# Kernel tuning notes

Hardware: AMD Instinct MI355X
Metric: run time of the kernel (lower is better)

Reference implementation:

```python
import jax, jax.numpy as jnp
import numpy as np

B, N, NG, K, H, C, BD = 4, 2048, 12, 16, 64, 128, 64
M = N // 4  # fps with down_sample=4
TWO_PI = 2.0 * np.pi


def _knn_idx(q, x, k):
    # q [Q,3] queries, x [P,3] pool -> [Q,k] indices of k nearest points in x
    d2 = jnp.sum((q[:, None, :] - x[None, :, :]) ** 2, axis=-1)
    _, idx = jax.lax.top_k(-d2, k)
    return idx


def _fps_idx(pos, m):
    # farthest point sampling, fixed m points, start at index 0
    n = pos.shape[0]
    def body(carry, _):
        d, last = carry
        dist = jnp.sum((pos - pos[last]) ** 2, axis=-1)
        d = jnp.minimum(d, dist)
        return (d, jnp.argmax(d)), last
    (_, _), idx = jax.lax.scan(body, (jnp.full((n,), 1e10, pos.dtype), jnp.int32(0)), None, length=m)
    return idx


def _basis_mlp(z, rff_w, w1, b1, w2, b2):
    # RFF -> Linear -> GELU -> Linear -> GELU
    p = TWO_PI * (z @ rff_w)
    f = jnp.concatenate([jnp.sin(p), jnp.cos(p)], axis=-1)
    h = jax.nn.gelu(f @ w1 + b1)
    return jax.nn.gelu(h @ w2 + b2)


def _interaction(x, nbr, kbx, kbR, kx_w, kx_b, kR_w, kR_b, mix_w, mix_b):
    # depthwise separable group conv: spatial gather-multiply-mean, then orientation mix
    kx = kbx @ kx_w + kx_b                     # [M,K,NG,C] spatial depthwise kernel
    kR = kbR @ kR_w + kR_b                     # [NG,NG,C] orientation depthwise kernel
    agg = jnp.mean(x[nbr] * kx, axis=1)        # [M,NG,C] mean over K neighbors
    y = jnp.einsum('bnc,mnc->bmc', agg, kR) / kR.shape[0]
    return x + jax.nn.gelu(y @ mix_w + mix_b)


def setup_inputs():
    key = jax.random.key(0)
    ks = iter(jax.random.split(key, 64))
    def randn(shape, std=1.0):
        return std * jax.random.normal(next(ks), shape, dtype=jnp.float32)
    inp = {}
    inp['pos'] = jax.random.uniform(next(ks), (B, N, 3), dtype=jnp.float32)
    nrm = randn((B, N, 3))
    inp['normal'] = nrm / jnp.linalg.norm(nrm, axis=-1, keepdims=True)
    g = randn((NG, 3))
    inp['grid'] = g / jnp.linalg.norm(g, axis=-1, keepdims=True)
    def lin(name, fin, fout):
        inp[name + '_w'] = randn((fin, fout), 1.0 / np.sqrt(fin))
        inp[name + '_b'] = jnp.zeros((fout,), jnp.float32)
    lin('emb1', 4, H); lin('emb2', H, H)
    lin('down', H, C)
    inp['bx_rff'] = randn((2, C // 2), 10.0)   # sigma=10
    lin('bx1', C, C); lin('bx2', C, BD)
    inp['bR_rff'] = randn((1, C // 2), 10.0)
    lin('bR1', C, C); lin('bR2', C, BD)
    for j in ('i1', 'i2'):
        lin(j + '_kx', BD, C); lin(j + '_kR', BD, C); lin(j + '_mix', C, C)
    lin('post1', C, 256); lin('post2', 256, 64); lin('post3', 64, 1)
    return inp


def reference(pos, normal, grid, emb1_w, emb1_b, emb2_w, emb2_b, down_w, down_b,
              bx_rff, bx1_w, bx1_b, bx2_w, bx2_b, bR_rff, bR1_w, bR1_b, bR2_w, bR2_b,
              i1_kx_w, i1_kx_b, i1_kR_w, i1_kR_b, i1_mix_w, i1_mix_b,
              i2_kx_w, i2_kx_b, i2_kR_w, i2_kR_b, i2_mix_w, i2_mix_b,
              post1_w, post1_b, post2_w, post2_b, post3_w, post3_b):
    def per_graph(p, nm):
        # lift: fiber features = <grid, normal> plus broadcast positions -> [N,NG,4]
        feat = jnp.concatenate([(nm @ grid.T)[:, :, None],
                                jnp.broadcast_to(p[:, None, :], (p.shape[0], NG, 3))], axis=-1)
        x = jax.nn.gelu(feat @ emb1_w + emb1_b) @ emb2_w + emb2_b   # [N,NG,H]
        # downsample block: fps + knn + linear/relu + scatter-max (exactly K edges per target)
        sel = _fps_idx(p, M)
        nbr_d = _knn_idx(p[sel], p, K)                               # [M,K] into N
        h = jax.nn.relu(x @ down_w + down_b)                         # [N,NG,C]
        x = jnp.max(h[nbr_d], axis=1)                                # [M,NG,C]
        ps = p[sel]
        # convolver block: knn graph + r3s2 edge attrs + basis MLPs + 2 interaction layers
        nbr = _knn_idx(ps, ps, K)                                    # [M,K] into M
        rel = ps[nbr] - ps[:, None, :]                               # pos[src]-pos[tgt], [M,K,3]
        rz = jnp.einsum('mke,ne->mkn', rel, grid)                    # [M,K,NG]
        rxy = jnp.sqrt(jnp.sum((rel[:, :, None, :] - rz[..., None] * grid) ** 2, axis=-1) + 1e-12)
        rpx = jnp.stack([rxy, rz], axis=-1)                          # [M,K,NG,2]
        rpR = (grid @ grid.T)[:, :, None]                            # [NG,NG,1]
        kbx = _basis_mlp(rpx, bx_rff, bx1_w, bx1_b, bx2_w, bx2_b)    # [M,K,NG,BD]
        kbR = _basis_mlp(rpR, bR_rff, bR1_w, bR1_b, bR2_w, bR2_b)    # [NG,NG,BD]
        x = _interaction(x, nbr, kbx, kbR, i1_kx_w, i1_kx_b, i1_kR_w, i1_kR_b, i1_mix_w, i1_mix_b)
        x = _interaction(x, nbr, kbx, kbR, i2_kx_w, i2_kx_b, i2_kR_w, i2_kR_b, i2_mix_w, i2_mix_b)
        # readout: mean over grid, global mean pool, MLP head
        g = jnp.mean(x, axis=(0, 1))                                 # [C]
        h1 = jax.nn.gelu(g @ post1_w + post1_b)
        h2 = jax.nn.gelu(h1 @ post2_w + post2_b)
        return h2 @ post3_w + post3_b                                # [1]
    return jax.vmap(per_graph)(pos, normal)                          # [B,1]
```

## Files before the change

### kernel.cpp

```cpp
#include <hip/hip_runtime.h>
#include <hip/hip_bf16.h>
#include <cfloat>

#define B_ 4
#define N_ 2048
#define NG_ 12
#define K_ 16
#define H_ 64
#define C_ 128
#define BD_ 64
#define M_ 512

typedef __attribute__((ext_vector_type(8))) short short8;
typedef __attribute__((ext_vector_type(4))) float floatx4;
typedef unsigned short ushort_t;
typedef unsigned int uint_t;

__device__ __forceinline__ float gelu_f(float x){
  float s = 0.7978845608028654f*(x + 0.044715f*x*x*x);
  float e = __expf(2.0f*s);
  float t = 1.0f - 2.0f/(e + 1.0f);
  return 0.5f*x*(1.0f + t);
}

__device__ __forceinline__ ushort_t bf16_rne(float x){
  uint_t u = __float_as_uint(x);
  uint_t r = (u + 0x7fffu + ((u >> 16) & 1u)) >> 16;
  return (ushort_t)r;
}

__device__ __forceinline__ uint_t pack_hl(float x){
  ushort_t hi = bf16_rne(x);
  float hif = __uint_as_float(((uint_t)hi)<<16);
  ushort_t lo = bf16_rne(x - hif);
  return (uint_t)hi | ((uint_t)lo << 16);
}

__device__ __forceinline__ uint_t cvtpk_bf16(float a, float b){
  uint_t r;
  asm("v_cvt_pk_bf16_f32 %0, %1, %2" : "=v"(r) : "v"(a), "v"(b));
  return r;
}

__device__ __forceinline__ void split2(float v0, float v1, uint_t& hp, uint_t& lp){
  hp = cvtpk_bf16(v0, v1);
  float h0 = __uint_as_float(hp << 16);
  float h1 = __uint_as_float(hp & 0xffff0000u);
  lp = cvtpk_bf16(v0 - h0, v1 - h1);
}

__device__ __forceinline__ uint_t pack_hl2(float v){
  uint_t hp = cvtpk_bf16(v, v);
  float hf = __uint_as_float(hp << 16);
  uint_t lp = cvtpk_bf16(v - hf, v - hf);
  return (hp & 0xffffu) | (lp << 16);
}

__device__ __forceinline__ uint_t perm_lo16(uint_t a, uint_t b){ return __builtin_amdgcn_perm(a, b, 0x05040100u); }
__device__ __forceinline__ uint_t perm_hi16(uint_t a, uint_t b){ return __builtin_amdgcn_perm(a, b, 0x07060302u); }

#define UNPACK8(Q0, Q1, AH, AL) { \
  uint_t* _ap = (uint_t*)&(AH); uint_t* _lp = (uint_t*)&(AL); \
  _ap[0] = perm_lo16((Q0).y, (Q0).x); _ap[1] = perm_lo16((Q0).w, (Q0).z); \
  _ap[2] = perm_lo16((Q1).y, (Q1).x); _ap[3] = perm_lo16((Q1).w, (Q1).z); \
  _lp[0] = perm_hi16((Q0).y, (Q0).x); _lp[1] = perm_hi16((Q0).w, (Q0).z); \
  _lp[2] = perm_hi16((Q1).y, (Q1).x); _lp[3] = perm_hi16((Q1).w, (Q1).z); }

#define DPP_AMAX(CTRL) { \
  int _vb = __float_as_int(v); \
  int _ov = __builtin_amdgcn_update_dpp(_vb, _vb, (CTRL), 0xF, 0xF, false); \
  int _oi = __builtin_amdgcn_update_dpp(vi, vi, (CTRL), 0xF, 0xF, false); \
  float _of = __int_as_float(_ov); \
  bool _tk = (_of > v) || (_of == v && _oi < vi); \
  v = _tk ? _of : v; vi = _tk ? _oi : vi; }

#define DPP_AMIN(CTRL) { \
  int _vb = __float_as_int(v); \
  int _ov = __builtin_amdgcn_update_dpp(_vb, _vb, (CTRL), 0xF, 0xF, false); \
  int _oi = __builtin_amdgcn_update_dpp(vi, vi, (CTRL), 0xF, 0xF, false); \
  float _of = __int_as_float(_ov); \
  bool _tk = (_of < v) || (_of == v && _oi < vi); \
  v = _tk ? _of : v; vi = _tk ? _oi : vi; }

#define FPSB 4
#define LIFTB (B_*N_*NG_/4)
#define WSB 64
#define KBRB (NG_*NG_)
#define PM4B 32
#define AKB (B_*N_/4)

__global__ __launch_bounds__(256) void k_mega1(
    const float* __restrict__ pos, const float* __restrict__ normal,
    const float* __restrict__ grid,
    const float* __restrict__ e1w, const float* __restrict__ e1b,
    const float* __restrict__ e2w, const float* __restrict__ e2b,
    uint_t* __restrict__ x1p, float* __restrict__ ps,
    float4* __restrict__ pos4, float4* __restrict__ ps4,
    int* __restrict__ sidxG, int* __restrict__ allD,
    const float* __restrict__ bx1w, const float* __restrict__ bx2w,
    const float* __restrict__ kxw1, const float* __restrict__ kxw2,
    const float* __restrict__ dww,
    ushort_t* __restrict__ w1hiT, ushort_t* __restrict__ w1loT,
    ushort_t* __restrict__ w2hiT, ushort_t* __restrict__ w2loT,
    ushort_t* __restrict__ x1hiT, ushort_t* __restrict__ x1loT,
    ushort_t* __restrict__ x2hiT, ushort_t* __restrict__ x2loT,
    ushort_t* __restrict__ dwThi, ushort_t* __restrict__ dwTlo,
    const float* __restrict__ bR_rff,
    const float* __restrict__ bR1w, const float* __restrict__ bR1b,
    const float* __restrict__ bR2w, const float* __restrict__ bR2b,
    const float* __restrict__ kR1w, const float* __restrict__ kR1b,
    const float* __restrict__ kR2w, const float* __restrict__ kR2b,
    float* __restrict__ kRb1, float* __restrict__ kRb2){
  __shared__ float4 posS4[N_];
  __shared__ float2 wred[2][4];
  __shared__ int sidxS[M_];
  __shared__ float ts4[4][64];
  __shared__ float fsb[128], hsb[128];
  int bid = blockIdx.x;
  int tid = threadIdx.x;

  if (bid < FPSB){
    int b = bid;
    for (int i=tid;i<N_;i+=256){
      const float* p = pos + (size_t)b*N_*3 + (size_t)i*3;
      posS4[i] = make_float4(p[0], p[1], p[2], 0.f);
    }
    __syncthreads();
    float px[8],py[8],pz[8],d[8];
    #pragma unroll
    for (int j=0;j<8;++j){
      float4 pt = posS4[tid + 256*j];
      px[j]=pt.x; py[j]=pt.y; pz[j]=pt.z;
      d[j]=1e10f;
    }
    int wave = tid>>6, lane = tid&63;
    int last = 0;
    for (int s=0;s<M_;++s){
      if (tid==0) sidxS[s] = last;
      if (s==M_-1) break;
      float4 lp = posS4[last];
      float lx=lp.x, ly=lp.y, lz=lp.z;
      #pragma unroll
      for (int j=0;j<8;++j){
        float dx=__fsub_rn(px[j],lx), dy=__fsub_rn(py[j],ly), dz=__fsub_rn(pz[j],lz);
        float dist=__fadd_rn(__fadd_rn(__fmul_rn(dx,dx),__fmul_rn(dy,dy)),__fmul_rn(dz,dz));
        d[j]=fminf(d[j],dist);
      }
      float va = d[1]>d[0]?d[1]:d[0]; int ja = d[1]>d[0]?1:0;
      float vb = d[3]>d[2]?d[3]:d[2]; int jb = d[3]>d[2]?3:2;
      float vc = d[5]>d[4]?d[5]:d[4]; int jc = d[5]>d[4]?5:4;
      float vd = d[7]>d[6]?d[7]:d[6]; int jd = d[7]>d[6]?7:6;
      float ve = vb>va?vb:va; int je = vb>va?jb:ja;
      float vf = vd>vc?vd:vc; int jf = vd>vc?jd:jc;
      float v  = vf>ve?vf:ve; int jj = vf>ve?jf:je;
      int vi = tid + (jj<<8);
      DPP_AMAX(0x121); DPP_AMAX(0x122); DPP_AMAX(0x124); DPP_AMAX(0x128);
      DPP_AMAX(0x142); DPP_AMAX(0x143);
      int sv = __builtin_amdgcn_readlane(__float_as_int(v), 63);
      int si = __builtin_amdgcn_readlane(vi, 63);
      if (lane==0) wred[s&1][wave] = make_float2(__int_as_float(sv), __int_as_float(si));
      __syncthreads();
      float2 r0 = wred[s&1][0], r1 = wred[s&1][1], r2 = wred[s&1][2], r3 = wred[s&1][3];
      float bv = r0.x; int bi = __float_as_int(r0.y);
      int i1 = __float_as_int(r1.y); if (r1.x>bv || (r1.x==bv && i1<bi)){ bv=r1.x; bi=i1; }
      int i2 = __float_as_int(r2.y); if (r2.x>bv || (r2.x==bv && i2<bi)){ bv=r2.x; bi=i2; }
      int i3 = __float_as_int(r3.y); if (r3.x>bv || (r3.x==bv && i3<bi)){ bv=r3.x; bi=i3; }
      last = bi;
    }
    __syncthreads();
    for (int i=tid; i<M_; i+=256){
      int si = sidxS[i];
      float4 p = posS4[si];
      float* o = ps + ((size_t)b*M_+i)*3;
      o[0]=p.x; o[1]=p.y; o[2]=p.z;
      ps4[(size_t)b*M_+i] = make_float4(p.x, p.y, p.z, 0.f);
      sidxG[(size_t)b*M_+i] = si;
    }
  } else if (bid < FPSB + LIFTB){
    int vbid = bid - FPSB;
    int q = tid>>6, lane = tid&63;
    int fid = vbid*4 + q;
    int g = fid % NG_;
    int n = (fid / NG_) % N_;
    int b = fid / (NG_*N_);
    const float* nm = normal + (size_t)(b*N_+n)*3;
    const float* pp = pos + (size_t)(b*N_+n)*3;
    const float* gg = grid + g*3;
    float f0 = nm[0]*gg[0] + nm[1]*gg[1] + nm[2]*gg[2];
    float t = e1b[lane] + f0*e1w[lane] + pp[0]*e1w[64+lane] + pp[1]*e1w[128+lane] + pp[2]*e1w[192+lane];
    ts4[q][lane] = gelu_f(t);
    __syncthreads();
    float acc = e2b[lane];
    #pragma unroll
    for (int i=0;i<64;++i) acc = fmaf(ts4[q][i], e2w[i*64+lane], acc);
    x1p[(size_t)fid*64 + lane] = pack_hl(acc);
  } else if (bid < FPSB + LIFTB + WSB){
    int tg = (bid - FPSB - LIFTB)*256 + tid;
    if (tg < 16384){
      int j = tg >> 7, k = tg & 127;
      float x = bx1w[k*128 + j];
      ushort_t hi = bf16_rne(x);
      float hif = __uint_as_float(((uint_t)hi)<<16);
      ushort_t lo = bf16_rne(x - hif);
      w1hiT[tg] = hi; w1loT[tg] = lo;
    }
    if (tg < 8192){
      int c = tg >> 7, j = tg & 127;
      float x = bx2w[j*64 + c];
      ushort_t hi = bf16_rne(x);
      float hif = __uint_as_float(((uint_t)hi)<<16);
      ushort_t lo = bf16_rne(x - hif);
      w2hiT[tg] = hi; w2loT[tg] = lo;
    }
    if (tg < 8192){
      int c = tg >> 6, d = tg & 63;
      float xa = kxw1[d*128 + c];
      ushort_t hi = bf16_rne(xa);
      float hif = __uint_as_float(((uint_t)hi)<<16);
      ushort_t lo = bf16_rne(xa - hif);
      x1hiT[tg] = hi; x1loT[tg] = lo;
      float xb = kxw2[d*128 + c];
      ushort_t hi2 = bf16_rne(xb);
      float hif2 = __uint_as_float(((uint_t)hi2)<<16);
      ushort_t lo2 = bf16_rne(xb - hif2);
      x2hiT[tg] = hi2; x2loT[tg] = lo2;
      float xd = dww[d*128 + c];
      ushort_t hi3 = bf16_rne(xd);
      float hif3 = __uint_as_float(((uint_t)hi3)<<16);
      ushort_t lo3 = bf16_rne(xd - hif3);
      dwThi[tg] = hi3; dwTlo[tg] = lo3;
    }
  } else if (bid < FPSB + LIFTB + WSB + KBRB){
    int vbid = bid - FPSB - LIFTB - WSB;
    int gm = vbid / NG_, gn = vbid % NG_;
    int j = tid;
    if (j < 128){
      float z = grid[gm*3]*grid[gn*3] + grid[gm*3+1]*grid[gn*3+1] + grid[gm*3+2]*grid[gn*3+2];
      float ang = 6.283185307179586f * (z * bR_rff[j & 63]);
      fsb[j] = (j<64) ? sinf(ang) : cosf(ang);
    }
    __syncthreads();
    if (j < 128){
      float acc = bR1b[j];
      for (int i=0;i<128;++i) acc = fmaf(fsb[i], bR1w[i*128+j], acc);
      hsb[j] = gelu_f(acc);
    }
    __syncthreads();
    if (j < 64){
      float a2 = bR2b[j];
      for (int i=0;i<128;++i) a2 = fmaf(hsb[i], bR2w[i*64+j], a2);
      fsb[j] = gelu_f(a2);
    }
    __syncthreads();
    if (j < 128){
      float a1 = kR1b[j], a2v = kR2b[j];
      for (int d=0; d<64; ++d){
        float kv = fsb[d];
        a1  = fmaf(kv, kR1w[d*128+j], a1);
        a2v = fmaf(kv, kR2w[d*128+j], a2v);
      }
      kRb1[(size_t)vbid*128 + j] = a1;
      kRb2[(size_t)vbid*128 + j] = a2v;
    }
  } else if (bid < FPSB + LIFTB + WSB + KBRB + PM4B){
    int i = (bid - FPSB - LIFTB - WSB - KBRB)*256 + tid;
    const float* p = pos + (size_t)i*3;
    pos4[i] = make_float4(p[0], p[1], p[2], 0.f);
  } else {
    int w = tid>>6, lane = tid&63;
    int qi = (bid - FPSB - LIFTB - WSB - KBRB - PM4B)*4 + w;
    int b = qi / N_;
    const float* q = pos + (size_t)qi*3;
    float qx=q[0], qy=q[1], qz=q[2];
    float d2[32];
    #pragma unroll
    for (int j=0;j<32;++j){
      const float* p = pos + ((size_t)(b*N_) + lane + 64*j)*3;
      float dx=__fsub_rn(qx,p[0]), dy=__fsub_rn(qy,p[1]), dz=__fsub_rn(qz,p[2]);
      d2[j]=__fadd_rn(__fadd_rn(__fmul_rn(dx,dx),__fmul_rn(dy,dy)),__fmul_rn(dz,dz));
    }
    for (int r=0;r<K_;++r){
      float v=FLT_MAX; int vi=0x7fffffff;
      #pragma unroll
      for (int j=0;j<32;++j){
        if (d2[j]<v){ v=d2[j]; vi=lane+64*j; }
      }
      DPP_AMIN(0x121); DPP_AMIN(0x122); DPP_AMIN(0x124); DPP_AMIN(0x128);
      DPP_AMIN(0x142); DPP_AMIN(0x143);
      int si = __builtin_amdgcn_readlane(vi, 63);
      if (lane==0) allD[(size_t)qi*K_ + r] = si;
      #pragma unroll
      for (int j=0;j<32;++j){ if (si == lane + 64*j) d2[j] = FLT_MAX; }
    }
  }
}

template<int NP>
__device__ __forceinline__ void knn_body4(int qm, const float4* __restrict__ qp4,
                                          const float4* __restrict__ pool4, int* __restrict__ out){
  constexpr int R = NP/64;
  int lane = threadIdx.x & 63;
  int b = qm / M_;
  float4 q = qp4[qm];
  float qx=q.x, qy=q.y, qz=q.z;
  float d2[R];
  #pragma unroll
  for (int j=0;j<R;++j){
    float4 p = pool4[(size_t)b*NP + lane + 64*j];
    float dx=__fsub_rn(qx,p.x), dy=__fsub_rn(qy,p.y), dz=__fsub_rn(qz,p.z);
    d2[j]=__fadd_rn(__fadd_rn(__fmul_rn(dx,dx),__fmul_rn(dy,dy)),__fmul_rn(dz,dz));
  }
  for (int r=0;r<K_;++r){
    float v=FLT_MAX; int vi=0x7fffffff;
    #pragma unroll
    for (int j=0;j<R;++j){
      if (d2[j]<v){ v=d2[j]; vi=lane+64*j; }
    }
    DPP_AMIN(0x121); DPP_AMIN(0x122); DPP_AMIN(0x124); DPP_AMIN(0x128);
    DPP_AMIN(0x142); DPP_AMIN(0x143);
    int si = __builtin_amdgcn_readlane(vi, 63);
    if (lane==0) out[(size_t)qm*K_ + r] = si;
    #pragma unroll
    for (int j=0;j<R;++j){ if (si == lane + 64*j) d2[j] = FLT_MAX; }
  }
}

__global__ __launch_bounds__(256) void k_knn_all(const float4* __restrict__ ps4,
    int* __restrict__ nbrS){
  int w = threadIdx.x >> 6;
  knn_body4<M_>(blockIdx.x*4 + w, ps4, ps4, nbrS);
}

__device__ __forceinline__ void dm_body(uint_t* um, int bm,
    const uint_t* __restrict__ x1p,
    const int* __restrict__ sidxG, const int* __restrict__ allD,
    const ushort_t* __restrict__ dwThi, const ushort_t* __restrict__ dwTlo,
    const float* __restrict__ db, float* __restrict__ xA){
  int b = bm / M_;
  int tid = threadIdx.x;
  uint_t* xs = um;
  int* nb = (int*)(um + 12288);
  if (tid < K_) nb[tid] = allD[((size_t)(b*N_) + sidxG[bm])*K_ + tid];
  __syncthreads();
  for (int idx=tid; idx<3072; idx+=256){
    int k = idx / 192, qq = idx % 192;
    uint4 vv = ((const uint4*)&x1p[((size_t)(b*N_) + nb[k])*(NG_*H_)])[qq];
    int gran = (qq >> 1) ^ (k & 7);
    *(uint4*)&xs[k*768 + gran*8 + (qq&1)*4] = vv;
  }
  __syncthreads();
  int wid = tid>>6, lane = tid&63, ln = lane&15, g4 = lane>>4;
  short8 bh[2][2], bl[2][2];
  float dbv[2];
  #pragma unroll
  for (int nt=0; nt<2; ++nt){
    int col = wid*32 + nt*16 + ln;
    dbv[nt] = db[col];
    #pragma unroll
    for (int ks=0; ks<2; ++ks){
      bh[nt][ks] = *(const short8*)&dwThi[(size_t)col*64 + ks*32 + g4*8];
      bl[nt][ks] = *(const short8*)&dwTlo[(size_t)col*64 + ks*32 + g4*8];
    }
  }
  int xorl = ln & 7;
  #pragma unroll
  for (int g=0; g<NG_; ++g){
    short8 ah[2], al[2];
    #pragma unroll
    for (int ks=0; ks<2; ++ks){
      int col0 = g*64 + ks*32 + g4*8;
      int gran = (col0 >> 3) ^ xorl;
      const uint_t* src = &xs[ln*768 + gran*8];
      uint4 q0 = *(const uint4*)src;
      uint4 q1 = *(const uint4*)(src+4);
      UNPACK8(q0, q1, ah[ks], al[ks]);
    }
    floatx4 acc[2];
    acc[0] = (floatx4){0.f,0.f,0.f,0.f};
    acc[1] = (floatx4){0.f,0.f,0.f,0.f};
    #pragma unroll
    for (int nt=0; nt<2; ++nt)
      #pragma unroll
      for (int ks=0; ks<2; ++ks){
        acc[nt] = __builtin_amdgcn_mfma_f32_16x16x32_bf16(ah[ks], bh[nt][ks], acc[nt], 0,0,0);
        acc[nt] = __builtin_amdgcn_mfma_f32_16x16x32_bf16(al[ks], bh[nt][ks], acc[nt], 0,0,0);
        acc[nt] = __builtin_amdgcn_mfma_f32_16x16x32_bf16(ah[ks], bl[nt][ks], acc[nt], 0,0,0);
      }
    #pragma unroll
    for (int nt=0; nt<2; ++nt){
      float mx = fmaxf(fmaxf(acc[nt][0],acc[nt][1]), fmaxf(acc[nt][2],acc[nt][3]));
      mx = fmaxf(mx, __shfl_xor(mx, 16));
      mx = fmaxf(mx, __shfl_xor(mx, 32));
      if (g4 == 0)
        xA[(size_t)bm*(NG_*C_) + g*C_ + wid*32 + nt*16 + ln] = fmaxf(mx + dbv[nt], 0.0f);
    }
  }
}

__device__ __forceinline__ void kbx_body(float* um, int vbid,
    const float* __restrict__ ps, const int* __restrict__ nbr,
    const float* __restrict__ grid, const float* __restrict__ rff,
    const ushort_t* __restrict__ w1hiT, const ushort_t* __restrict__ w1loT,
    const ushort_t* __restrict__ w2hiT, const ushort_t* __restrict__ w2loT,
    const float* __restrict__ b1, const float* __restrict__ b2,
    uint_t* __restrict__ kbxp){
  float* z0s = um;
  float* z1s = um + 128;
  float* rws = um + 256;
  int tid = threadIdx.x;
  if (tid < 128){
    rws[tid] = rff[tid];
    int fid = vbid*128 + tid;
    int g = fid % NG_;
    int k = (fid/NG_) % K_;
    int bm = fid / (NG_*K_);
    int b = bm / M_;
    int nb = nbr[(size_t)bm*K_ + k];
    const float* pm = ps + (size_t)bm*3;
    const float* pn = ps + ((size_t)(b*M_) + nb)*3;
    float rx = pn[0]-pm[0], ry = pn[1]-pm[1], rz3 = pn[2]-pm[2];
    const float* gg = grid + g*3;
    float rz = rx*gg[0] + ry*gg[1] + rz3*gg[2];
    float vx = rx - rz*gg[0], vy = ry - rz*gg[1], vz = rz3 - rz*gg[2];
    float rxy = sqrtf(vx*vx + vy*vy + vz*vz + 1e-12f);
    z0s[tid]=rxy; z1s[tid]=rz;
  }
  __syncthreads();
  int wid = tid>>6, lane = tid&63;
  int ln = lane & 15, g = lane >> 4;
  float* bw = um + 384 + wid*1088;

  short8 ahi[2][4], alo[2][4];
  #pragma unroll
  for (int rt=0; rt<2; ++rt){
    float z0 = z0s[wid*32 + rt*16 + ln];
    float z1 = z1s[wid*32 + rt*16 + ln];
    #pragma unroll
    for (int ks=0; ks<4; ++ks){
      float vv[8];
      #pragma unroll
      for (int e=0; e<8; ++e){
        int kd = ks*32 + g*8 + e;
        int kk = kd & 63;
        float t = z0*rws[kk] + z1*rws[64+kk];
        t = t - floorf(t);
        vv[e] = (ks < 2) ? __builtin_amdgcn_sinf(t) : __builtin_amdgcn_cosf(t);
      }
      uint_t* hp = (uint_t*)&ahi[rt][ks];
      uint_t* lp = (uint_t*)&alo[rt][ks];
      #pragma unroll
      for (int p=0; p<4; ++p) split2(vv[2*p], vv[2*p+1], hp[p], lp[p]);
    }
  }
  floatx4 acc2[2][4];
  #pragma unroll
  for (int rt=0; rt<2; ++rt)
    #pragma unroll
    for (int ct=0; ct<4; ++ct)
      acc2[rt][ct] = (floatx4){0.f,0.f,0.f,0.f};

  #pragma unroll
  for (int jp=0; jp<4; ++jp){
    floatx4 acc1[2][2];
    #pragma unroll
    for (int rt=0; rt<2; ++rt)
      #pragma unroll
      for (int jt=0; jt<2; ++jt)
        acc1[rt][jt] = (floatx4){0.f,0.f,0.f,0.f};
    #pragma unroll
    for (int ks=0; ks<4; ++ks){
      #pragma unroll
      for (int jt=0; jt<2; ++jt){
        int j = jp*32 + jt*16 + ln;
        short8 bhi = *(const short8*)&w1hiT[(size_t)j*128 + ks*32 + g*8];
        short8 blo = *(const short8*)&w1loT[(size_t)j*128 + ks*32 + g*8];
        #pragma unroll
        for (int rt=0; rt<2; ++rt){
          acc1[rt][jt] = __builtin_amdgcn_mfma_f32_16x16x32_bf16(ahi[rt][ks], bhi, acc1[rt][jt], 0,0,0);
          acc1[rt][jt] = __builtin_amdgcn_mfma_f32_16x16x32_bf16(alo[rt][ks], bhi, acc1[rt][jt], 0,0,0);
          acc1[rt][jt] = __builtin_amdgcn_mfma_f32_16x16x32_bf16(ahi[rt][ks], blo, acc1[rt][jt], 0,0,0);
        }
      }
    }
    #pragma unroll
    for (int jt=0; jt<2; ++jt){
      float bb = b1[jp*32 + jt*16 + ln];
      #pragma unroll
      for (int rt=0; rt<2; ++rt)
        #pragma unroll
        for (int i=0; i<4; ++i)
          bw[(rt*16 + g*4 + i)*34 + jt*16 + ln] = gelu_f(bb + acc1[rt][jt][i]);
    }
    #pragma unroll
    for (int rt=0; rt<2; ++rt){
      int base = (rt*16 + ln)*34 + g*8;
      float2 p0 = *(float2*)&bw[base+0];
      float2 p1 = *(float2*)&bw[base+2];
      float2 p2 = *(float2*)&bw[base+4];
      float2 p3 = *(float2*)&bw[base+6];
      short8 a2h, a2l;
      uint_t* hp = (uint_t*)&a2h;
      uint_t* lp = (uint_t*)&a2l;
      split2(p0.x, p0.y, hp[0], lp[0]);
      split2(p1.x, p1.y, hp[1], lp[1]);
      split2(p2.x, p2.y, hp[2], lp[2]);
      split2(p3.x, p3.y, hp[3], lp[3]);
      #pragma unroll
      for (int ct=0; ct<4; ++ct){
        short8 b2h = *(const short8*)&w2hiT[(size_t)(ct*16+ln)*128 + jp*32 + g*8];
        short8 b2l = *(const short8*)&w2loT[(size_t)(ct*16+ln)*128 + jp*32 + g*8];
        acc2[rt][ct] = __builtin_amdgcn_mfma_f32_16x16x32_bf16(a2h, b2h, acc2[rt][ct], 0,0,0);
        acc2[rt][ct] = __builtin_amdgcn_mfma_f32_16x16x32_bf16(a2l, b2h, acc2[rt][ct], 0,0,0);
        acc2[rt][ct] = __builtin_amdgcn_mfma_f32_16x16x32_bf16(a2h, b2l, acc2[rt][ct], 0,0,0);
      }
    }
  }
  #pragma unroll
  for (int ct=0; ct<4; ++ct){
    float bb = b2[ct*16 + ln];
    #pragma unroll
    for (int rt=0; rt<2; ++rt)
      #pragma unroll
      for (int i=0; i<4; ++i){
        int row = wid*32 + rt*16 + g*4 + i;
        size_t fiber = (size_t)vbid*128 + row;
        kbxp[fiber*64 + ct*16 + ln] = pack_hl2(gelu_f(bb + acc2[rt][ct][i]));
      }
  }
}

__global__ __launch_bounds__(256) void k_dmkbx(
    const uint_t* __restrict__ x1p,
    const int* __restrict__ sidxG, const int* __restrict__ allD,
    const ushort_t* __restrict__ dwThi, const ushort_t* __restrict__ dwTlo,
    const float* __restrict__ db, float* __restrict__ xA,
    const float* __restrict__ ps, const int* __restrict__ nbrS,
    const float* __restrict__ grid, const float* __restrict__ rff,
    const ushort_t* __restrict__ w1hiT, const ushort_t* __restrict__ w1loT,
    const ushort_t* __restrict__ w2hiT, const ushort_t* __restrict__ w2loT,
    const float* __restrict__ b1, const float* __restrict__ b2,
    uint_t* __restrict__ kbxp){
  __shared__ __align__(16) uint_t um[12384];
  int bid = blockIdx.x;
  if (bid < B_*M_)
    dm_body(um, bid, x1p, sidxG, allD, dwThi, dwTlo, db, xA);
  else
    kbx_body((float*)um, bid - B_*M_, ps, nbrS, grid, rff, w1hiT, w1loT, w2hiT, w2loT, b1, b2, kbxp);
}

__global__ __launch_bounds__(256) void k_inter(
    const float* __restrict__ xin, const int* __restrict__ nbr,
    const uint_t* __restrict__ kbxp, const float* __restrict__ kR,
    const ushort_t* __restrict__ kxhT, const ushort_t* __restrict__ kxlT,
    const float* __restrict__ kxb,
    const float* __restrict__ mw, const float* __restrict__ mb,
    float* __restrict__ xout, float* __restrict__ part){
  int bm = blockIdx.x; int b = bm / M_;
  int tid = threadIdx.x;
  int wid = tid>>6, lane = tid&63, ln = lane&15, g4 = lane>>4;
  int c = tid & 127, gh = tid >> 7;
  __shared__ uint_t kbsL[48][68];
  __shared__ __align__(16) float TsU[48*129];
  float* aggS_ = TsU;
  float* yS_   = TsU + 1536;
  float* psumS_= TsU + 3072;

  const uint4* ksrc = (const uint4*)(kbxp + (size_t)bm*192*64);

  uint4 ka = ksrc[tid], kbv = ksrc[tid+256], kc = ksrc[tid+512];
  int nb0 = nbr[(size_t)bm*K_+0], nb1 = nbr[(size_t)bm*K_+1],
      nb2 = nbr[(size_t)bm*K_+2], nb3 = nbr[(size_t)bm*K_+3];

  short8 bh[2][2], bl[2][2];
  float kxbv[2];
  #pragma unroll
  for (int nt=0; nt<2; ++nt){
    int cc_ = (wid*2+nt)*16 + ln;
    kxbv[nt] = kxb[cc_];
    #pragma unroll
    for (int ks=0; ks<2; ++ks){
      bh[nt][ks] = *(const short8*)&kxhT[(size_t)cc_*64 + ks*32 + g4*8];
      bl[nt][ks] = *(const short8*)&kxlT[(size_t)cc_*64 + ks*32 + g4*8];
    }
  }
  float accg[6] = {0,0,0,0,0,0};

  for (int cc=0; cc<4; ++cc){
    {
      int i0=tid, i1=tid+256, i2=tid+512;
      *(uint4*)&kbsL[i0>>4][(i0&15)*4] = ka;
      *(uint4*)&kbsL[i1>>4][(i1&15)*4] = kbv;
      *(uint4*)&kbsL[i2>>4][(i2&15)*4] = kc;
    }
    __syncthreads();
    float xreg[24];
    {
      const float* xr0 = xin + ((size_t)(b*M_) + nb0)*(NG_*C_);
      const float* xr1 = xin + ((size_t)(b*M_) + nb1)*(NG_*C_);
      const float* xr2 = xin + ((size_t)(b*M_) + nb2)*(NG_*C_);
      const float* xr3 = xin + ((size_t)(b*M_) + nb3)*(NG_*C_);
      #pragma unroll
      for (int gi=0; gi<6; ++gi){
        int off = (gh*6+gi)*C_ + c;
        xreg[0*6+gi] = xr0[off];
        xreg[1*6+gi] = xr1[off];
        xreg[2*6+gi] = xr2[off];
        xreg[3*6+gi] = xr3[off];
      }
    }
    if (cc < 3){
      ka  = ksrc[(cc+1)*768 + tid];
      kbv = ksrc[(cc+1)*768 + tid + 256];
      kc  = ksrc[(cc+1)*768 + tid + 512];
      nb0 = nbr[(size_t)bm*K_ + (cc+1)*4 + 0];
      nb1 = nbr[(size_t)bm*K_ + (cc+1)*4 + 1];
      nb2 = nbr[(size_t)bm*K_ + (cc+1)*4 + 2];
      nb3 = nbr[(size_t)bm*K_ + (cc+1)*4 + 3];
    }
    floatx4 acc[3][2];
    #pragma unroll
    for (int mt=0; mt<3; ++mt)
      #pragma unroll
      for (int nt=0; nt<2; ++nt)
        acc[mt][nt] = (floatx4){0.f,0.f,0.f,0.f};
    #pragma unroll
    for (int mt=0; mt<3; ++mt){
      short8 ah[2], al[2];
      #pragma unroll
      for (int ks=0; ks<2; ++ks){
        const uint_t* src = &kbsL[mt*16+ln][ks*32+g4*8];
        uint4 q0 = *(const uint4*)src;
        uint4 q1 = *(const uint4*)(src+4);
        UNPACK8(q0, q1, ah[ks], al[ks]);
      }
      #pragma unroll
      for (int nt=0; nt<2; ++nt)
        #pragma unroll
        for (int ks=0; ks<2; ++ks){
          acc[mt][nt] = __builtin_amdgcn_mfma_f32_16x16x32_bf16(ah[ks], bh[nt][ks], acc[mt][nt], 0,0,0);
          acc[mt][nt] = __builtin_amdgcn_mfma_f32_16x16x32_bf16(al[ks], bh[nt][ks], acc[mt][nt], 0,0,0);
          acc[mt][nt] = __builtin_amdgcn_mfma_f32_16x16x32_bf16(ah[ks], bl[nt][ks], acc[mt][nt], 0,0,0);
        }
    }
    #pragma unroll
    for (int mt=0; mt<3; ++mt)
      #pragma unroll
      for (int nt=0; nt<2; ++nt)
        #pragma unroll
        for (int i=0; i<4; ++i)
          TsU[(mt*16 + g4*4 + i)*129 + (wid*2+nt)*16 + ln] = acc[mt][nt][i] + kxbv[nt];
    __syncthreads();
    #pragma unroll
    for (int kl=0; kl<4; ++kl)
      #pragma unroll
      for (int gi=0; gi<6; ++gi)
        accg[gi] = fmaf(TsU[(kl*12 + gh*6 + gi)*129 + c], xreg[kl*6+gi], accg[gi]);
    __syncthreads();
  }
  #pragma unroll
  for (int gi=0; gi<6; ++gi)
    aggS_[(gh*6+gi)*C_ + c] = accg[gi] * (1.0f/16.0f);
  __syncthreads();
  #pragma unroll
  for (int gi=0; gi<6; ++gi){
    int g = gh*6+gi;
    float yv = 0.f;
    #pragma unroll
    for (int n=0;n<NG_;++n) yv = fmaf(aggS_[n*C_ + c], kR[((size_t)g*NG_+n)*C_ + c], yv);
    yS_[g*C_ + c] = yv * (1.0f/12.0f);
  }
  __syncthreads();
  float m6[6] = {0,0,0,0,0,0};
  for (int i4=0;i4<32;++i4){
    float w0 = mw[(i4*4+0)*C_+c], w1 = mw[(i4*4+1)*C_+c],
          w2 = mw[(i4*4+2)*C_+c], w3 = mw[(i4*4+3)*C_+c];
    #pragma unroll
    for (int gi=0;gi<6;++gi){
      int g = gh*6+gi;
      float4 yv = *(const float4*)&yS_[g*C_ + i4*4];
      m6[gi] = fmaf(yv.x,w0,fmaf(yv.y,w1,fmaf(yv.z,w2,fmaf(yv.w,w3,m6[gi]))));
    }
  }
  float mbc = mb[c];
  float psum = 0.f;
  #pragma unroll
  for (int gi=0;gi<6;++gi){
    int g = gh*6+gi;
    size_t off = (size_t)bm*(NG_*C_) + g*C_ + c;
    float val = xin[off] + gelu_f(m6[gi] + mbc);
    xout[off] = val;
    psum += val;
  }
  if (part){
    psumS_[gh*C_ + c] = psum;
    __syncthreads();
    if (gh == 0)
      part[(size_t)bm*C_ + c] = psumS_[c] + psumS_[C_ + c];
  }
}

__global__ __launch_bounds__(256) void k_head(
    const float* __restrict__ part,
    const float* __restrict__ p1w, const float* __restrict__ p1b,
    const float* __restrict__ p2w, const float* __restrict__ p2b,
    const float* __restrict__ p3w, const float* __restrict__ p3b,
    float* __restrict__ out){
  int b = blockIdx.x, tid = threadIdx.x;
  int c = tid & 127, half = tid >> 7;
  __shared__ float red[256];
  __shared__ float gs[128];
  {
    const float* pb = part + (size_t)b*M_*C_;
    float a0=0.f,a1=0.f,a2=0.f,a3=0.f;
    for (int r = half*4; r < M_; r += 8){
      a0 += pb[(size_t)(r+0)*C_ + c];
      a1 += pb[(size_t)(r+1)*C_ + c];
      a2 += pb[(size_t)(r+2)*C_ + c];
      a3 += pb[(size_t)(r+3)*C_ + c];
    }
    red[tid] = (a0+a1)+(a2+a3);
  }
  __syncthreads();
  if (half==0) gs[c] = (red[c] + red[128+c]) * (1.0f/(M_*NG_));
  __syncthreads();
  __shared__ float h1[256];
  {
    float a = p1b[tid];
    for (int i=0;i<128;++i) a = fmaf(gs[i], p1w[i*256+tid], a);
    h1[tid] = gelu_f(a);
  }
  __syncthreads();
  __shared__ float h2[64];
  if (tid<64){
    float a = p2b[tid];
    for (int i=0;i<256;++i) a = fmaf(h1[i], p2w[i*64+tid], a);
    h2[tid] = gelu_f(a);
  }
  __syncthreads();
  if (tid==0){
    float a = p3b[0];
    for (int i=0;i<64;++i) a = fmaf(h2[i], p3w[i], a);
    out[b] = a;
  }
}

extern "C" void kernel_launch(void* const* d_in, const int* in_sizes, int n_in,
                              void* d_out, int out_size, void* d_ws, size_t ws_size,
                              hipStream_t stream){
  const float* pos    = (const float*)d_in[0];
  const float* normal = (const float*)d_in[1];
  const float* grid   = (const float*)d_in[2];
  const float* e1w = (const float*)d_in[3];  const float* e1b = (const float*)d_in[4];
  const float* e2w = (const float*)d_in[5];  const float* e2b = (const float*)d_in[6];
  const float* dww = (const float*)d_in[7];  const float* dwb = (const float*)d_in[8];
  const float* bx_rff = (const float*)d_in[9];
  const float* bx1w = (const float*)d_in[10]; const float* bx1b = (const float*)d_in[11];
  const float* bx2w = (const float*)d_in[12]; const float* bx2b = (const float*)d_in[13];
  const float* bR_rff = (const float*)d_in[14];
  const float* bR1w = (const float*)d_in[15]; const float* bR1b = (const float*)d_in[16];
  const float* bR2w = (const float*)d_in[17]; const float* bR2b = (const float*)d_in[18];
  const float* i1kxw = (const float*)d_in[19]; const float* i1kxb = (const float*)d_in[20];
  const float* i1kRw = (const float*)d_in[21]; const float* i1kRb = (const float*)d_in[22];
  const float* i1mw  = (const float*)d_in[23]; const float* i1mb  = (const float*)d_in[24];
  const float* i2kxw = (const float*)d_in[25]; const float* i2kxb = (const float*)d_in[26];
  const float* i2kRw = (const float*)d_in[27]; const float* i2kRb = (const float*)d_in[28];
  const float* i2mw  = (const float*)d_in[29]; const float* i2mb  = (const float*)d_in[30];
  const float* p1w = (const float*)d_in[31]; const float* p1b = (const float*)d_in[32];
  const float* p2w = (const float*)d_in[33]; const float* p2b = (const float*)d_in[34];
  const float* p3w = (const float*)d_in[35]; const float* p3b = (const float*)d_in[36];
  float* out = (float*)d_out;

  float* ws = (float*)d_ws;
  size_t o = 0;
  uint_t* x1p = (uint_t*)(ws + o); o += (size_t)B_*N_*NG_*H_;
  float* psb = ws + o; o += (size_t)B_*M_*3;
  float* xA  = ws + o; o += (size_t)B_*M_*NG_*C_;
  float* xB  = ws + o; o += (size_t)B_*M_*NG_*C_;
  uint_t* kbxp = (uint_t*)(ws + o); o += (size_t)B_*M_*K_*NG_*BD_;
  float* kRb1 = ws + o; o += (size_t)NG_*NG_*C_;
  float* kRb2 = ws + o; o += (size_t)NG_*NG_*C_;
  float* part = ws + o; o += (size_t)B_*M_*C_;
  float4* pos4 = (float4*)(ws + o); o += (size_t)B_*N_*4;
  float4* ps4  = (float4*)(ws + o); o += (size_t)B_*M_*4;
  int* sidxG = (int*)(ws + o); o += (size_t)B_*M_;
  int* allD  = (int*)(ws + o); o += (size_t)B_*N_*K_;
  int* nbrS  = (int*)(ws + o); o += (size_t)B_*M_*K_;
  ushort_t* w1hiT = (ushort_t*)(ws + o); o += 8192;
  ushort_t* w1loT = (ushort_t*)(ws + o); o += 8192;
  ushort_t* w2hiT = (ushort_t*)(ws + o); o += 4096;
  ushort_t* w2loT = (ushort_t*)(ws + o); o += 4096;
  ushort_t* x1hiT = (ushort_t*)(ws + o); o += 4096;
  ushort_t* x1loT = (ushort_t*)(ws + o); o += 4096;
  ushort_t* x2hiT = (ushort_t*)(ws + o); o += 4096;
  ushort_t* x2loT = (ushort_t*)(ws + o); o += 4096;
  ushort_t* dwThi = (ushort_t*)(ws + o); o += 4096;
  ushort_t* dwTlo = (ushort_t*)(ws + o); o += 4096;

  k_mega1<<<FPSB + LIFTB + WSB + KBRB + PM4B + AKB, 256, 0, stream>>>(
      pos, normal, grid, e1w, e1b, e2w, e2b, x1p, psb, pos4, ps4, sidxG, allD,
      bx1w, bx2w, i1kxw, i2kxw, dww,
      w1hiT, w1loT, w2hiT, w2loT, x1hiT, x1loT, x2hiT, x2loT, dwThi, dwTlo,
      bR_rff, bR1w, bR1b, bR2w, bR2b,
      i1kRw, i1kRb, i2kRw, i2kRb, kRb1, kRb2);
  k_knn_all<<<B_*M_/4, 256, 0, stream>>>(ps4, nbrS);
  k_dmkbx<<<B_*M_ + (B_*M_*K_*NG_)/128, 256, 0, stream>>>(
      x1p, sidxG, allD, dwThi, dwTlo, dwb, xA,
      psb, nbrS, grid, bx_rff, w1hiT, w1loT, w2hiT, w2loT, bx1b, bx2b, kbxp);
  k_inter<<<B_*M_, 256, 0, stream>>>(xA, nbrS, kbxp, kRb1, x1hiT, x1loT, i1kxb, i1mw, i1mb, xB, nullptr);
  k_inter<<<B_*M_, 256, 0, stream>>>(xB, nbrS, kbxp, kRb2, x2hiT, x2loT, i2kxb, i2mw, i2mb, xA, part);
  k_head<<<B_, 256, 0, stream>>>(part, p1w, p1b, p2w, p2b, p3w, p3b, out);
}
```

Baseline: 722.7 us.

## Load dm neighbor rows directly from global and drop shared staging

The downsample-max body no longer stages the 16 neighbor feature rows in shared memory. Each MFMA step now loads one neighbor's row straight from global memory, with the grid index on the lane axis, and keeps a running max over neighbors in registers. That removes two barriers and the shared-memory footprint, so the fused kernel's LDS drops and more blocks can be resident per CU. Block order is also swapped so the kbx blocks come first. The cost is repeated uncoalesced global reads of the neighbor rows and padded lanes (12 of 16 rows used) that do wasted MFMA work.

Result: slower. 798.5 us (+10.5%).

```diff
diff --git a/kernel.cpp b/kernel.cpp
--- a/kernel.cpp
+++ b/kernel.cpp
@@ -331,25 +331,16 @@
   knn_body4<M_>(blockIdx.x*4 + w, ps4, ps4, nbrS);
 }
 
-__device__ __forceinline__ void dm_body(uint_t* um, int bm,
+__device__ __forceinline__ void dm_body(int bm,
     const uint_t* __restrict__ x1p,
     const int* __restrict__ sidxG, const int* __restrict__ allD,
     const ushort_t* __restrict__ dwThi, const ushort_t* __restrict__ dwTlo,
     const float* __restrict__ db, float* __restrict__ xA){
   int b = bm / M_;
   int tid = threadIdx.x;
-  uint_t* xs = um;
-  int* nb = (int*)(um + 12288);
-  if (tid < K_) nb[tid] = allD[((size_t)(b*N_) + sidxG[bm])*K_ + tid];
-  __syncthreads();
-  for (int idx=tid; idx<3072; idx+=256){
-    int k = idx / 192, qq = idx % 192;
-    uint4 vv = ((const uint4*)&x1p[((size_t)(b*N_) + nb[k])*(NG_*H_)])[qq];
-    int gran = (qq >> 1) ^ (k & 7);
-    *(uint4*)&xs[k*768 + gran*8 + (qq&1)*4] = vv;
-  }
-  __syncthreads();
   int wid = tid>>6, lane = tid&63, ln = lane&15, g4 = lane>>4;
+  int lnc = (ln < NG_) ? ln : 0;
+  const int* nbp = allD + ((size_t)(b*N_) + sidxG[bm])*K_;
   short8 bh[2][2], bl[2][2];
   float dbv[2];
   #pragma unroll
@@ -362,15 +353,19 @@
       bl[nt][ks] = *(const short8*)&dwTlo[(size_t)col*64 + ks*32 + g4*8];
     }
   }
-  int xorl = ln & 7;
-  #pragma unroll
-  for (int g=0; g<NG_; ++g){
+  float mx[2][4];
+  #pragma unroll
+  for (int nt=0; nt<2; ++nt)
+    #pragma unroll
+    for (int i=0; i<4; ++i) mx[nt][i] = -FLT_MAX;
+  #pragma unroll
+  for (int k=0; k<K_; ++k){
+    int nb = nbp[k];
+    const uint_t* row = x1p + ((size_t)(b*N_) + nb)*(NG_*H_);
     short8 ah[2], al[2];
     #pragma unroll
     for (int ks=0; ks<2; ++ks){
-      int col0 = g*64 + ks*32 + g4*8;
-      int gran = (col0 >> 3) ^ xorl;
-      const uint_t* src = &xs[ln*768 + gran*8];
+      const uint_t* src = row + lnc*64 + ks*32 + g4*8;
       uint4 q0 = *(const uint4*)src;
       uint4 q1 = *(const uint4*)(src+4);
       UNPACK8(q0, q1, ah[ks], al[ks]);
@@ -387,13 +382,19 @@
         acc[nt] = __builtin_amdgcn_mfma_f32_16x16x32_bf16(ah[ks], bl[nt][ks], acc[nt], 0,0,0);
       }
     #pragma unroll
-    for (int nt=0; nt<2; ++nt){
-      float mx = fmaxf(fmaxf(acc[nt][0],acc[nt][1]), fmaxf(acc[nt][2],acc[nt][3]));
-      mx = fmaxf(mx, __shfl_xor(mx, 16));
-      mx = fmaxf(mx, __shfl_xor(mx, 32));
-      if (g4 == 0)
-        xA[(size_t)bm*(NG_*C_) + g*C_ + wid*32 + nt*16 + ln] = fmaxf(mx + dbv[nt], 0.0f);
-    }
+    for (int nt=0; nt<2; ++nt)
+      #pragma unroll
+      for (int i=0; i<4; ++i)
+        mx[nt][i] = fmaxf(mx[nt][i], acc[nt][i]);
+  }
+  if (g4 < 3){
+    #pragma unroll
+    for (int nt=0; nt<2; ++nt)
+      #pragma unroll
+      for (int i=0; i<4; ++i){
+        int g = g4*4 + i;
+        xA[(size_t)bm*(NG_*C_) + g*C_ + wid*32 + nt*16 + ln] = fmaxf(mx[nt][i] + dbv[nt], 0.0f);
+      }
   }
 }
 
@@ -529,6 +530,8 @@
   }
 }
 
+#define KBXB ((B_*M_*K_*NG_)/128)
+
 __global__ __launch_bounds__(256) void k_dmkbx(
     const uint_t* __restrict__ x1p,
     const int* __restrict__ sidxG, const int* __restrict__ allD,
@@ -540,12 +543,13 @@
     const ushort_t* __restrict__ w2hiT, const ushort_t* __restrict__ w2loT,
     const float* __restrict__ b1, const float* __restrict__ b2,
     uint_t* __restrict__ kbxp){
-  __shared__ __align__(16) uint_t um[12384];
+  __shared__ __align__(16) float um[4736];
   int bid = blockIdx.x;
-  if (bid < B_*M_)
-    dm_body(um, bid, x1p, sidxG, allD, dwThi, dwTlo, db, xA);
+  int nkbx = (B_*M_*K_*NG_)/128;
+  if (bid < nkbx)
+    kbx_body(um, bid, ps, nbrS, grid, rff, w1hiT, w1loT, w2hiT, w2loT, b1, b2, kbxp);
   else
-    kbx_body((float*)um, bid - B_*M_, ps, nbrS, grid, rff, w1hiT, w1loT, w2hiT, w2loT, b1, b2, kbxp);
+    dm_body(bid - nkbx, x1p, sidxG, allD, dwThi, dwTlo, db, xA);
 }
 
 __global__ __launch_bounds__(256) void k_inter(
```
